# Kernel optimization log

Measured on AMD Instinct MI355X. Metric: run time of the kernel, lower is better.

The kernel has to match this reference:

```python
import jax, jax.numpy as jnp
import numpy as np
from jax import lax

# ---------- patch unfold/fold for kernel k = 2*stride (CP1: k=4,s=2; CP2: k=16,s=8) ----------

def _unfold2(x, s):
    # extract (2s x 2s) patches, stride s, VALID; x: [b,c,H,W] with H,W multiples of s
    b, c, H, W = x.shape
    nh, nw = H // s - 1, W // s - 1
    xv = x.reshape(b, c, H // s, s, W // s, s)
    quads = jnp.stack([xv[:, :, qh:qh + nh, :, qw:qw + nw, :]
                       for qh in (0, 1) for qw in (0, 1)], axis=2)
    # (b,c,q,nh,u,nw,v) -> (b,nh,nw,c,q,u,v)
    p = quads.transpose(0, 3, 5, 1, 2, 4, 6)
    return p.reshape(b, nh * nw, c * 4 * s * s), (nh, nw)


def _fold2(contrib, nh, nw, c, s):
    # overlap-add inverse of _unfold2; contrib: [b, nh*nw, c*4*s*s]
    b = contrib.shape[0]
    cr = contrib.reshape(b, nh, nw, c, 2, 2, s, s)
    out = jnp.zeros((b, c, nh + 1, s, nw + 1, s), contrib.dtype)
    for qh in (0, 1):
        for qw in (0, 1):
            blk = cr[:, :, :, :, qh, qw].transpose(0, 3, 1, 4, 2, 5)  # [b,c,nh,s,nw,s]
            out = out.at[:, :, qh:qh + nh, :, qw:qw + nw, :].add(blk)
    return out.reshape(b, c, (nh + 1) * s, (nw + 1) * s)

# ---------- gated conv (gen_conv2) / nearest-up + gated conv (gen_deconv2) ----------

def _gconv(x, w, b, stride=1, act='elu'):
    k = w.shape[-1]
    p = (k - 1) // 2
    y = lax.conv_general_dilated(x, w, (stride, stride), [(p, p), (p, p)],
                                 dimension_numbers=('NCHW', 'OIHW', 'NCHW'))
    y = y + b[None, :, None, None]
    if w.shape[0] == 3 or act is None:
        return y
    a, g = jnp.split(y, 2, axis=1)
    a = jax.nn.relu(a) if act == 'relu' else jax.nn.elu(a)
    return a * jax.nn.sigmoid(g)


def _gdeconv(x, w, b):
    x = jnp.repeat(jnp.repeat(x, 2, axis=2), 2, axis=3)  # nearest x2
    return _gconv(x, w, b)

# ---------- CP1: patch cosine-correlation + softmax matching ----------

def _cp1(x1, x2, mask, pd=1, s=2, scale=10.0):
    pads = ((0, 0), (0, 0), (pd, pd), (pd, pd))
    q, (nh, nw) = _unfold2(jnp.pad(x1, pads), s)   # [b,L,P] query patches
    kpat, _ = _unfold2(jnp.pad(x2, pads), s)       # [b,L,P] background (key) patches
    mpat, _ = _unfold2(jnp.pad(mask, pads), s)     # [b,L,4*s*s]
    kn = kpat / jnp.maximum(jnp.linalg.norm(kpat, axis=-1, keepdims=True), 1e-4)
    mm = (jnp.mean(mpat, axis=-1) == 0.).astype(x1.dtype)  # 1 = fully-known bkg patch
    cos = jnp.einsum('bqp,blp->blq', q, kn) * mm[:, :, None]
    sim = jax.nn.softmax(cos * scale, axis=1) * mm[:, :, None]
    b = x1.shape[0]
    return sim.reshape(b, nh * nw, nh, nw)

# ---------- CP2: weighted patch paste (transposed-conv reconstruction) ----------

def _cp2(sim, xb, mask, pd=4, s=8):
    b, c, H, W = xb.shape
    w, (nh, nw) = _unfold2(jnp.pad(xb, ((0, 0), (0, 0), (pd, pd), (pd, pd))), s)
    L = nh * nw
    simf = sim.reshape(b, L, L)                       # [b, L_key, L_query]
    contrib = jnp.einsum('blq,blp->bqp', simf, w)     # weighted patch per query loc
    out = _fold2(contrib, nh, nw, c, s)
    cnt = _fold2(jnp.ones((b, L, 4 * s * s), xb.dtype), nh, nw, 1, s)
    out = out / jnp.maximum(cnt, 1e-8)                # overlap average
    out = out[:, :, pd:pd + H, pd:pd + W]
    return out * mask + xb * (1. - mask)


def setup_inputs() -> dict:
    key = jax.random.key(0)
    ks = iter(jax.random.split(key, 64))
    B, H, W, cnum = 4, 256, 256, 48
    x = jax.random.uniform(next(ks), (B, 3, H, W), jnp.float32, -1., 1.)
    x_stage1 = jax.random.uniform(next(ks), (B, 3, H, W), jnp.float32, -1., 1.)
    x_stage2 = jax.random.uniform(next(ks), (B, 3, H, W), jnp.float32, -1., 1.)
    mask = jnp.zeros((B, 1, H, W), jnp.float32).at[:, :, 64:192, 64:192].set(1.)  # box hole
    pm = jax.random.normal(next(ks), (B, 2 * cnum, H // 4, W // 4), jnp.float32)
    inp = dict(x=x, mask=mask, x_stage1=x_stage1, x_stage2=x_stage2, pm=pm)
    specs = [('sconv1', 4 * cnum, 2 * cnum, 5), ('sconv2', 4 * cnum, 2 * cnum, 3),
             ('bconv1', cnum, 3, 5), ('bconv2', 2 * cnum, cnum // 2, 3),
             ('bconv3', 2 * cnum, cnum, 3), ('bconv4', 4 * cnum, cnum, 3),
             ('conv13', 2 * cnum, 2 * cnum, 3), ('conv14', 2 * cnum, 2 * cnum, 3),
             ('conv15', cnum, cnum, 3), ('conv16', cnum, cnum, 3),
             ('conv16_2', cnum, cnum // 2, 3), ('conv17', 3, cnum // 2, 3)]
    for name, cout, cin, kk in specs:
        inp['w_' + name] = jax.random.normal(next(ks), (cout, cin, kk, kk), jnp.float32) * 0.05
        inp['b_' + name] = jnp.zeros((cout,), jnp.float32)
    return inp


def reference(x, mask, x_stage1, x_stage2, pm,
              w_sconv1, b_sconv1, w_sconv2, b_sconv2,
              w_bconv1, b_bconv1, w_bconv2, b_bconv2,
              w_bconv3, b_bconv3, w_bconv4, b_bconv4,
              w_conv13, b_conv13, w_conv14, b_conv14,
              w_conv15, b_conv15, w_conv16, b_conv16,
              w_conv16_2, b_conv16_2, w_conv17, b_conv17):
    xnow = x_stage2 * mask + x * (1. - mask)
    xs = _gconv(pm, w_sconv1, b_sconv1)                       # [B,96,64,64]
    x_similar = _gconv(xs, w_sconv2, b_sconv2, act='relu')    # [B,96,64,64]
    B, _, Hm, Wm = mask.shape
    mask_s = mask.reshape(B, 1, Hm // 4, 4, Wm // 4, 4).mean(axis=(3, 5))  # avg_pool 4x4
    similar = _cp1(x_similar, x_similar, mask_s)              # [B,1024,32,32]
    xb = _gconv(xnow, w_bconv1, b_bconv1)
    skip1 = xb
    xb = _gconv(xb, w_bconv2, b_bconv2, stride=2)
    xb = _gconv(xb, w_bconv3, b_bconv3)
    skip2 = xb
    xb = _gconv(xb, w_bconv4, b_bconv4, stride=2)
    xb = _gdeconv(xb, w_conv13, b_conv13)
    xb = _gconv(jnp.concatenate([xb, skip2], axis=1), w_conv14, b_conv14)
    xb = _gdeconv(xb, w_conv15, b_conv15)
    xb = _gconv(jnp.concatenate([xb, skip1], axis=1), w_conv16, b_conv16)
    xb = _cp2(similar, xb, mask)                              # [B,24,256,256]
    xb = _gconv(xb, w_conv16_2, b_conv16_2)
    xb = jnp.tanh(_gconv(xb, w_conv17, b_conv17, act=None))
    return (x_stage1, x_stage2, xb)
```

## Files before the change

kernel.cpp:

```cpp
#include <hip/hip_runtime.h>
#include <math.h>

#define BB 4

typedef __bf16 bf16x8 __attribute__((ext_vector_type(8)));
typedef float f32x4 __attribute__((ext_vector_type(4)));

__device__ inline ushort f2bf(float x) {
  uint u = __float_as_uint(x);
  uint r = (u + 0x7fffu + ((u >> 16) & 1u)) >> 16;
  return (ushort)r;
}
__device__ inline float bf2f(ushort h) { return __uint_as_float(((uint)h) << 16); }
__device__ inline bf16x8 as_bf(uint4 u) {
  union { uint4 u; bf16x8 b; } c;
  c.u = u;
  return c.b;
}

struct WPtrs { const float* w[12]; };

#define WTOTAL 146560

__global__ void prep_w_all(WPtrs wp, uint4* __restrict__ wbH) {
  const int tK[12]    = {5,3,5,3,3,3,3,3,3,3,3,3};
  const int tCC[12]   = {8,16,8,8,16,8,16,16,16,16,8,8};
  const int tSP[12]   = {28,10,28,12,10,12,10,10,10,10,12,12};
  const int tcinR[12] = {96,96,3,24,48,48,96,96,48,48,24,24};
  const int tcinp[12] = {96,96,8,24,48,48,96,96,48,48,24,24};
  const int tcout[12] = {96,96,24,48,48,96,48,48,24,24,24,3};
  const int tgat[12]  = {1,1,1,1,1,1,1,1,1,1,1,0};
  const int toff[13]  = {0,64512,87552,89344,92800,98560,112384,123904,135424,139264,143104,145408,146560};
  for (int i = blockIdx.x * 256 + threadIdx.x; i < WTOTAL; i += gridDim.x * 256) {
    int L = 0;
    while (toff[L + 1] <= i) L++;
    int li = i - toff[L];
    int K = tK[L], CC = tCC[L], SPAD = tSP[L];
    int CH = CC >> 3;
    int SZ = SPAD * CH * 32;
    int nch = tcinp[L] / CC;
    int yb = li / (nch * SZ);
    int rem = li - yb * nch * SZ;
    int chunk = rem / SZ;
    int t = rem - chunk * SZ;
    int ci0 = chunk * CC;
    int co32 = t & 31, sh = t >> 5;
    int s = sh / CH, hh = sh - s * CH;
    int fr;
    bool ok;
    if (tgat[L]) {
      int coL = yb * 16 + (co32 & 15);
      ok = coL < tcout[L];
      fr = (co32 < 16) ? coL : tcout[L] + coL;
    } else {
      fr = yb * 32 + co32;
      ok = fr < tcout[L];
    }
    ok = ok && (s < K * K);
    const float* wgt = wp.w[L];
    union { ushort u[8]; uint4 v; } th;
#pragma unroll
    for (int j = 0; j < 8; j++) {
      int ci = ci0 + hh * 8 + j;
      float v = 0.f;
      if (ok && ci < tcinR[L]) v = wgt[((size_t)fr * tcinR[L] + ci) * (K * K) + s];
      th.u[j] = f2bf(v);
    }
    wbH[i] = th.v;
  }
}

__global__ void k_xnow(const float* __restrict__ x, const float* __restrict__ x2,
                       const float* __restrict__ mask,
                       ushort* __restrict__ outH, ushort* __restrict__ outL) {
  int idx = blockIdx.x * 256 + threadIdx.x;
  if (idx >= BB * 65536) return;
  int b = idx >> 16, r = idx & 65535;
  float m = mask[idx];
  union { ushort u[8]; uint4 v; } h, l;
#pragma unroll
  for (int c = 0; c < 8; c++) { h.u[c] = 0; l.u[c] = 0; }
#pragma unroll
  for (int c = 0; c < 3; c++) {
    size_t s = ((size_t)(b * 3 + c) << 16) + r;
    float v = x2[s] * m + x[s] * (1.f - m);
    ushort hh = f2bf(v);
    h.u[c] = hh;
    l.u[c] = f2bf(v - bf2f(hh));
  }
  *(uint4*)&outH[(size_t)idx * 8] = h.v;
  *(uint4*)&outL[(size_t)idx * 8] = l.v;
}

__global__ void k_tr(const float* __restrict__ pm,
                     ushort* __restrict__ outH, ushort* __restrict__ outL) {
  int idx = blockIdx.x * 256 + threadIdx.x;
  if (idx >= BB * 4096) return;
  int b = idx >> 12, pix = idx & 4095;
#pragma unroll
  for (int g = 0; g < 12; g++) {
    union { ushort u[8]; uint4 v; } h, l;
#pragma unroll
    for (int j = 0; j < 8; j++) {
      float v = pm[(((size_t)b * 96 + g * 8 + j) << 12) + pix];
      ushort hh = f2bf(v);
      h.u[j] = hh;
      l.u[j] = f2bf(v - bf2f(hh));
    }
    *(uint4*)&outH[(size_t)idx * 96 + g * 8] = h.v;
    *(uint4*)&outL[(size_t)idx * 96 + g * 8] = l.v;
  }
}

template <int K, int STRIDE, int UP, int CC, int TH, int TW, int SPAD>
__global__ __launch_bounds__(256) void conv_mfma(
    const ushort* __restrict__ in1H, const ushort* __restrict__ in1L,
    const ushort* __restrict__ in2H, const ushort* __restrict__ in2L,
    int s1, int s2, int g1, int cinp,
    const uint4* __restrict__ wbH,
    const float* __restrict__ bias,
    ushort* __restrict__ outH, ushort* __restrict__ outL, float* __restrict__ outF,
    int Hin, int Win, int Hout, int Wout,
    int coutEff, int coutp, int act, int tilesX) {
  constexpr int CH = CC / 8;
  constexpr int GS = 4 / CH;
  constexpr int NGc = CC / 8;
  constexpr int CCp = (CC == 16) ? 24 : 8;
  constexpr int IH = (TH - 1) * STRIDE + K;
  constexpr int IW = (TW - 1) * STRIDE + K;
  constexpr int NF = (TH * TW) / 64;
  constexpr int NSC = SPAD / GS;
  constexpr int WSZ = SPAD * CH * 32;

  __shared__ ushort sInH[IH * IW * CCp];
  __shared__ ushort sInL[IH * IW * CCp];
  __shared__ uint4 sWH[WSZ];

  const int tid = threadIdx.x;
  const int lane = tid & 63, wv = tid >> 6;
  const int m = lane & 15, gg = lane >> 4;
  const int b = blockIdx.z;
  const int yb = blockIdx.y;
  const int tX = blockIdx.x % tilesX, tY = blockIdx.x / tilesX;
  const int pad = (K - 1) / 2;
  const int HinU = Hin << UP, WinU = Win << UP;
  const int oy0 = tY * TH * STRIDE - pad;
  const int ox0 = tX * TW * STRIDE - pad;
  const int gated = (act != 2);
  const int NG = cinp >> 3;
  const int nch = cinp / CC;
  const size_t HWin = (size_t)Hin * Win;

  f32x4 acc[2][NF];
#pragma unroll
  for (int i = 0; i < 2; i++)
#pragma unroll
    for (int j = 0; j < NF; j++) acc[i][j] = (f32x4){0.f, 0.f, 0.f, 0.f};

  for (int ci0 = 0; ci0 < cinp; ci0 += CC) {
    __syncthreads();
    for (int t = tid; t < IH * IW * NGc; t += 256) {
      int p = (NGc == 2) ? (t >> 1) : t;
      int g = (NGc == 2) ? (t & 1) : 0;
      int iy = p / IW, ix = p % IW;
      int gy = oy0 + iy, gx = ox0 + ix;
      int gi = (ci0 >> 3) + g;
      uint4 h = {0u, 0u, 0u, 0u}, l = {0u, 0u, 0u, 0u};
      if (gi < NG && gy >= 0 && gy < HinU && gx >= 0 && gx < WinU) {
        int sy = gy >> UP, sx = gx >> UP;
        size_t poff = (size_t)b * HWin + (size_t)sy * Win + sx;
        if (gi < g1) {
          size_t a = poff * s1 + gi * 8;
          h = *(const uint4*)&in1H[a];
          l = *(const uint4*)&in1L[a];
        } else {
          size_t a = poff * s2 + (gi - g1) * 8;
          h = *(const uint4*)&in2H[a];
          l = *(const uint4*)&in2L[a];
        }
      }
      int d = p * CCp + g * 8;
      *(uint4*)&sInH[d] = h;
      *(uint4*)&sInL[d] = l;
    }
    {
      const uint4* pH = wbH + ((size_t)yb * nch + (ci0 / CC)) * WSZ;
      for (int t = tid; t < WSZ; t += 256) sWH[t] = pH[t];
    }
    __syncthreads();
#pragma unroll
    for (int sc = 0; sc < NSC; sc++) {
      int sg = sc * GS + gg / CH;
      int hh = gg - (gg / CH) * CH;
      int s = (sg < K * K) ? sg : 0;
      int kh = s / K, kw = s - kh * K;
      bf16x8 ah[2], bh[NF], bl[NF];
#pragma unroll
      for (int mi = 0; mi < 2; mi++) {
        int ai = (sc * 4 + gg) * 32 + mi * 16 + m;
        ah[mi] = as_bf(sWH[ai]);
      }
#pragma unroll
      for (int ni = 0; ni < NF; ni++) {
        int pix = wv * (NF * 16) + ni * 16 + m;
        int py = pix >> 4, px = pix & 15;
        int li = ((py * STRIDE + kh) * IW + px * STRIDE + kw) * CCp + hh * 8;
        bh[ni] = as_bf(*(const uint4*)&sInH[li]);
        bl[ni] = as_bf(*(const uint4*)&sInL[li]);
      }
#pragma unroll
      for (int mi = 0; mi < 2; mi++)
#pragma unroll
        for (int ni = 0; ni < NF; ni++) {
          acc[mi][ni] = __builtin_amdgcn_mfma_f32_16x16x32_bf16(ah[mi], bh[ni], acc[mi][ni], 0, 0, 0);
          acc[mi][ni] = __builtin_amdgcn_mfma_f32_16x16x32_bf16(ah[mi], bl[ni], acc[mi][ni], 0, 0, 0);
        }
    }
  }
  const size_t HWout = (size_t)Hout * Wout;
  if (gated) {
    int co0 = yb * 16 + gg * 4;
    bool cov = co0 < coutEff;
    float bA[4], bG[4];
#pragma unroll
    for (int r = 0; r < 4; r++) {
      bA[r] = cov ? bias[co0 + r] : 0.f;
      bG[r] = cov ? bias[coutEff + co0 + r] : 0.f;
    }
#pragma unroll
    for (int ni = 0; ni < NF; ni++) {
      int pix = wv * (NF * 16) + ni * 16 + m;
      int py = pix >> 4, px = pix & 15;
      int gy = tY * TH + py, gx = tX * TW + px;
      if (!cov) continue;
      union { ushort u[4]; uint2 v; } oh, ol;
#pragma unroll
      for (int r = 0; r < 4; r++) {
        float a = acc[0][ni][r] + bA[r];
        float g = acc[1][ni][r] + bG[r];
        float aa = (act == 1) ? fmaxf(a, 0.f) : (a > 0.f ? a : expm1f(a));
        float o = aa * (1.f / (1.f + expf(-g)));
        ushort hh = f2bf(o);
        oh.u[r] = hh;
        ol.u[r] = f2bf(o - bf2f(hh));
      }
      size_t base = ((size_t)b * HWout + (size_t)gy * Wout + gx) * coutp + co0;
      *(uint2*)&outH[base] = oh.v;
      *(uint2*)&outL[base] = ol.v;
    }
  } else {
#pragma unroll
    for (int mi = 0; mi < 2; mi++)
#pragma unroll
      for (int ni = 0; ni < NF; ni++) {
        int pix = wv * (NF * 16) + ni * 16 + m;
        int py = pix >> 4, px = pix & 15;
        int gy = tY * TH + py, gx = tX * TW + px;
#pragma unroll
        for (int r = 0; r < 4; r++) {
          int co = yb * 32 + mi * 16 + gg * 4 + r;
          if (co >= coutEff) continue;
          float o = tanhf(acc[mi][ni][r] + bias[co]);
          outF[(size_t)(b * coutEff + co) * HWout + (size_t)gy * Wout + gx] = o;
        }
      }
  }
}

__global__ void k_mask_s(const float* __restrict__ mask, float* __restrict__ mask_s) {
  int idx = blockIdx.x * 256 + threadIdx.x;
  if (idx >= BB * 4096) return;
  int b = idx >> 12, r = idx & 4095;
  int i = r >> 6, j = r & 63;
  float s = 0.f;
  for (int u = 0; u < 4; u++)
    for (int v = 0; v < 4; v++)
      s += mask[(size_t)b * 65536 + (i * 4 + u) * 256 + (j * 4 + v)];
  mask_s[idx] = s * (1.f / 16.f);
}

__global__ void k_mm(const float* __restrict__ mask_s, float* __restrict__ mm) {
  int idx = blockIdx.x * 256 + threadIdx.x;
  if (idx >= BB * 1024) return;
  int b = idx >> 10, l = idx & 1023;
  int li = l >> 5, lj = l & 31;
  float s = 0.f;
  for (int dy = 0; dy < 4; dy++) {
    int row = 2 * li + dy - 1;
    if (row < 0 || row >= 64) continue;
    for (int dx = 0; dx < 4; dx++) {
      int col = 2 * lj + dx - 1;
      if (col < 0 || col >= 64) continue;
      s += mask_s[((size_t)b << 12) + row * 64 + col];
    }
  }
  mm[idx] = (s == 0.f) ? 1.f : 0.f;
}

__global__ __launch_bounds__(256) void extract_patches_bf(
    const ushort* __restrict__ xsH, const ushort* __restrict__ xsL,
    ushort* __restrict__ Phi, ushort* __restrict__ Plo) {
  int bl = blockIdx.x;
  int b = bl >> 10, l = bl & 1023;
  int li = l >> 5, lj = l & 31;
  __shared__ ushort sH[1536], sL[1536];
  int tid = threadIdx.x;
  for (int t = tid; t < 192; t += 256) {
    ((uint4*)sH)[t] = (uint4){0u, 0u, 0u, 0u};
    ((uint4*)sL)[t] = (uint4){0u, 0u, 0u, 0u};
  }
  __syncthreads();
  if (tid < 192) {
    int px = tid / 12, g = tid % 12;
    int dy = px >> 2, dx = px & 3;
    int row = 2 * li + dy - 1, col = 2 * lj + dx - 1;
    if (row >= 0 && row < 64 && col >= 0 && col < 64) {
      size_t a = ((((size_t)b << 12) + (row << 6) + col) * 96) + g * 8;
      union { uint4 v; ushort u[8]; } h, lo;
      h.v = *(const uint4*)&xsH[a];
      lo.v = *(const uint4*)&xsL[a];
#pragma unroll
      for (int j = 0; j < 8; j++) {
        int c = g * 8 + j;
        sH[c * 16 + px] = h.u[j];
        sL[c * 16 + px] = lo.u[j];
      }
    }
  }
  __syncthreads();
  size_t o = (size_t)bl * 1536;
  for (int t = tid; t < 192; t += 256) {
    ((uint4*)(Phi + o))[t] = ((uint4*)sH)[t];
    ((uint4*)(Plo + o))[t] = ((uint4*)sL)[t];
  }
}

__global__ void k_scale_bf(const ushort* __restrict__ Phi, const ushort* __restrict__ Plo,
                           const float* __restrict__ mm, float* __restrict__ scale) {
  int bl = blockIdx.x;
  const ushort* rh = Phi + (size_t)bl * 1536;
  const ushort* rl = Plo + (size_t)bl * 1536;
  int tid = threadIdx.x;
  float s = 0.f;
  for (int i = 0; i < 6; i++) {
    float v = bf2f(rh[tid + i * 256]) + bf2f(rl[tid + i * 256]);
    s += v * v;
  }
  __shared__ float red[256];
  red[tid] = s; __syncthreads();
  for (int t = 128; t > 0; t >>= 1) { if (tid < t) red[tid] += red[tid + t]; __syncthreads(); }
  if (tid == 0) scale[bl] = mm[bl] / fmaxf(sqrtf(red[0]), 1e-4f);
}

__global__ __launch_bounds__(512) void gemm_qk_mfma(
    const ushort* __restrict__ Phi, const ushort* __restrict__ Plo,
    const float* __restrict__ scale, float* __restrict__ S) {
  int b = blockIdx.z;
  int qTile = blockIdx.y * 128, lTile = blockIdx.x * 128;
  __shared__ uint4 sAh[512], sAl[512], sBh[512], sBl[512];

  int tid = threadIdx.x;
  int lane = tid & 63, w = tid >> 6;
  int wy = w >> 2, wx = w & 3;
  int m = lane & 15, gg = lane >> 4;

  f32x4 acc[4][2];
#pragma unroll
  for (int i = 0; i < 4; i++)
#pragma unroll
    for (int j = 0; j < 2; j++) acc[i][j] = (f32x4){0.f, 0.f, 0.f, 0.f};

  for (int k0 = 0; k0 < 1536; k0 += 32) {
    __syncthreads();
    {
      int r = tid >> 2, g = tid & 3;
      int slot = (r << 2) + (g ^ ((r >> 1) & 3));
      size_t aoff = ((size_t)(b * 1024 + qTile + r)) * 1536 + k0;
      size_t boff = ((size_t)(b * 1024 + lTile + r)) * 1536 + k0;
      sAh[slot] = ((const uint4*)(Phi + aoff))[g];
      sAl[slot] = ((const uint4*)(Plo + aoff))[g];
      sBh[slot] = ((const uint4*)(Phi + boff))[g];
      sBl[slot] = ((const uint4*)(Plo + boff))[g];
    }
    __syncthreads();
    bf16x8 ah[4], al[4], bh[2], bl[2];
#pragma unroll
    for (int i = 0; i < 4; i++) {
      int ra = wy * 64 + i * 16 + m;
      int sa = (ra << 2) + (gg ^ ((ra >> 1) & 3));
      ah[i] = as_bf(sAh[sa]);
      al[i] = as_bf(sAl[sa]);
    }
#pragma unroll
    for (int j = 0; j < 2; j++) {
      int rb = wx * 32 + j * 16 + m;
      int sb = (rb << 2) + (gg ^ ((rb >> 1) & 3));
      bh[j] = as_bf(sBh[sb]);
      bl[j] = as_bf(sBl[sb]);
    }
#pragma unroll
    for (int mi = 0; mi < 4; mi++)
#pragma unroll
      for (int ni = 0; ni < 2; ni++) {
        acc[mi][ni] = __builtin_amdgcn_mfma_f32_16x16x32_bf16(ah[mi], bh[ni], acc[mi][ni], 0, 0, 0);
        acc[mi][ni] = __builtin_amdgcn_mfma_f32_16x16x32_bf16(ah[mi], bl[ni], acc[mi][ni], 0, 0, 0);
        acc[mi][ni] = __builtin_amdgcn_mfma_f32_16x16x32_bf16(al[mi], bh[ni], acc[mi][ni], 0, 0, 0);
      }
  }

#pragma unroll
  for (int ni = 0; ni < 2; ni++) {
    int l = lTile + wx * 32 + ni * 16 + m;
    float sc = scale[b * 1024 + l];
#pragma unroll
    for (int mi = 0; mi < 4; mi++) {
      int q0 = qTile + wy * 64 + mi * 16 + gg * 4;
#pragma unroll
      for (int r = 0; r < 4; r++)
        S[((size_t)b * 1024 + q0 + r) * 1024 + l] = acc[mi][ni][r] * sc;
    }
  }
}

__global__ void softmax_rows_bf(const float* __restrict__ S, const float* __restrict__ mm,
                                ushort* __restrict__ Shi, ushort* __restrict__ Slo) {
  int q = blockIdx.x, b = blockIdx.y;
  const float* row = S + ((size_t)b * 1024 + q) * 1024;
  int tid = threadIdx.x;
  float v[4];
  float mx = -1e30f;
  for (int i = 0; i < 4; i++) { v[i] = row[tid + i * 256]; mx = fmaxf(mx, v[i]); }
  __shared__ float red[256];
  red[tid] = mx; __syncthreads();
  for (int s = 128; s > 0; s >>= 1) { if (tid < s) red[tid] = fmaxf(red[tid], red[tid + s]); __syncthreads(); }
  mx = red[0]; __syncthreads();
  float sum = 0.f;
  for (int i = 0; i < 4; i++) { v[i] = expf(10.f * (v[i] - mx)); sum += v[i]; }
  red[tid] = sum; __syncthreads();
  for (int s = 128; s > 0; s >>= 1) { if (tid < s) red[tid] += red[tid + s]; __syncthreads(); }
  sum = red[0];
  float inv = 1.f / sum;
  for (int i = 0; i < 4; i++) {
    int l = tid + i * 256;
    float p = v[i] * inv * mm[b * 1024 + l];
    ushort h = f2bf(p);
    size_t o = ((size_t)b * 1024 + q) * 1024 + l;
    Shi[o] = h;
    Slo[o] = f2bf(p - bf2f(h));
  }
}

__global__ __launch_bounds__(256) void k_prepW(
    const ushort* __restrict__ t16H,
    ushort* __restrict__ WtH, int b) {
  int u = blockIdx.x >> 5, li = blockIdx.x & 31;
  int row = 8 * li + u - 4;
  bool rv = (row >= 0 && row < 256);
  __shared__ ushort sH[256 * 24];
  int tid = threadIdx.x;
  for (int t = tid; t < 768; t += 256) {
    uint4 h = {0u, 0u, 0u, 0u};
    if (rv) h = *(const uint4*)&t16H[((size_t)b * 65536 + (row << 8)) * 24 + t * 8];
    ((uint4*)sH)[t] = h;
  }
  __syncthreads();
  for (int pr = tid; pr < 384; pr += 256) {
    int v = pr / 24, c = pr - (pr / 24) * 24;
    int p = (u * 16 + v) * 24 + c;
    union { ushort us[32]; uint4 q[4]; } oh;
#pragma unroll 8
    for (int lj = 0; lj < 32; lj++) {
      int col = 8 * lj + v - 4;
      oh.us[lj] = (col >= 0 && col < 256) ? sH[col * 24 + c] : (ushort)0;
    }
    size_t o = (size_t)p * 1024 + li * 32;
#pragma unroll
    for (int g = 0; g < 4; g++) *(uint4*)&WtH[o + g * 8] = oh.q[g];
  }
}

__global__ __launch_bounds__(512) void gemm_cp2_mfma(
    const ushort* __restrict__ Shi, const ushort* __restrict__ Slo,
    const ushort* __restrict__ Wthi,
    float* __restrict__ contrib, int b) {
  int qTile = blockIdx.y * 128, pTile = blockIdx.x * 128;
  __shared__ uint4 sAh[512], sAl[512], sBh[512];

  int tid = threadIdx.x;
  int lane = tid & 63, w = tid >> 6;
  int wy = w >> 2, wx = w & 3;
  int m = lane & 15, gg = lane >> 4;

  f32x4 acc[4][2];
#pragma unroll
  for (int i = 0; i < 4; i++)
#pragma unroll
    for (int j = 0; j < 2; j++) acc[i][j] = (f32x4){0.f, 0.f, 0.f, 0.f};

  for (int l0 = 0; l0 < 1024; l0 += 32) {
    __syncthreads();
    {
      int r = tid >> 2, g = tid & 3;
      int slot = (r << 2) + (g ^ ((r >> 1) & 3));
      size_t aoff = ((size_t)(b * 1024 + qTile + r)) * 1024 + l0;
      size_t boff = ((size_t)(pTile + r)) * 1024 + l0;
      sAh[slot] = ((const uint4*)(Shi + aoff))[g];
      sAl[slot] = ((const uint4*)(Slo + aoff))[g];
      sBh[slot] = ((const uint4*)(Wthi + boff))[g];
    }
    __syncthreads();
    bf16x8 ah[4], al[4], bh[2];
#pragma unroll
    for (int i = 0; i < 4; i++) {
      int ra = wy * 64 + i * 16 + m;
      int sa = (ra << 2) + (gg ^ ((ra >> 1) & 3));
      ah[i] = as_bf(sAh[sa]);
      al[i] = as_bf(sAl[sa]);
    }
#pragma unroll
    for (int j = 0; j < 2; j++) {
      int rb = wx * 32 + j * 16 + m;
      int sb = (rb << 2) + (gg ^ ((rb >> 1) & 3));
      bh[j] = as_bf(sBh[sb]);
    }
#pragma unroll
    for (int mi = 0; mi < 4; mi++)
#pragma unroll
      for (int ni = 0; ni < 2; ni++) {
        acc[mi][ni] = __builtin_amdgcn_mfma_f32_16x16x32_bf16(ah[mi], bh[ni], acc[mi][ni], 0, 0, 0);
        acc[mi][ni] = __builtin_amdgcn_mfma_f32_16x16x32_bf16(al[mi], bh[ni], acc[mi][ni], 0, 0, 0);
      }
  }

#pragma unroll
  for (int ni = 0; ni < 2; ni++) {
    int p = pTile + wx * 32 + ni * 16 + m;
#pragma unroll
    for (int mi = 0; mi < 4; mi++) {
      int q0 = qTile + wy * 64 + mi * 16 + gg * 4;
#pragma unroll
      for (int r = 0; r < 4; r++)
        contrib[(size_t)(q0 + r) * 6144 + p] = acc[mi][ni][r];
    }
  }
}

__global__ void k_fold(const float* __restrict__ contrib,
                       const ushort* __restrict__ t16H, const ushort* __restrict__ t16L,
                       const float* __restrict__ mask,
                       ushort* __restrict__ outH, ushort* __restrict__ outL, int b) {
  int r = blockIdx.x * 256 + threadIdx.x;
  if (r >= 65536) return;
  int Y = r >> 8, X = r & 255;
  int yp = Y + 4, xp = X + 4;
  int qis[2], qjs[2];
  int cy = 0, cx = 0;
  int qi1 = yp >> 3;
  if (qi1 - 1 >= 0) qis[cy++] = qi1 - 1;
  if (qi1 < 32) qis[cy++] = qi1;
  int qj1 = xp >> 3;
  if (qj1 - 1 >= 0) qjs[cx++] = qj1 - 1;
  if (qj1 < 32) qjs[cx++] = qj1;
  float sum[24];
#pragma unroll
  for (int c = 0; c < 24; c++) sum[c] = 0.f;
  for (int a = 0; a < cy; a++)
    for (int d = 0; d < cx; d++) {
      int qi = qis[a], qj = qjs[d];
      int u = yp - 8 * qi, v = xp - 8 * qj;
      const float4* cp = (const float4*)&contrib[(size_t)(qi * 32 + qj) * 6144 + (u * 16 + v) * 24];
#pragma unroll
      for (int g = 0; g < 6; g++) {
        float4 f = cp[g];
        sum[g * 4 + 0] += f.x;
        sum[g * 4 + 1] += f.y;
        sum[g * 4 + 2] += f.z;
        sum[g * 4 + 3] += f.w;
      }
    }
  float inv = 1.f / (float)(cy * cx);
  float m = mask[(size_t)b * 65536 + r];
  size_t a16 = ((size_t)b * 65536 + r) * 24;
#pragma unroll
  for (int g = 0; g < 3; g++) {
    union { uint4 v; ushort u[8]; } th, tl, oh, ol;
    th.v = *(const uint4*)&t16H[a16 + g * 8];
    tl.v = *(const uint4*)&t16L[a16 + g * 8];
#pragma unroll
    for (int j = 0; j < 8; j++) {
      float base = bf2f(th.u[j]) + bf2f(tl.u[j]);
      float res = sum[g * 8 + j] * inv * m + base * (1.f - m);
      ushort h = f2bf(res);
      oh.u[j] = h;
      ol.u[j] = f2bf(res - bf2f(h));
    }
    *(uint4*)&outH[a16 + g * 8] = oh.v;
    *(uint4*)&outL[a16 + g * 8] = ol.v;
  }
}

extern "C" void kernel_launch(void* const* d_in, const int* in_sizes, int n_in,
                              void* d_out, int out_size, void* d_ws, size_t ws_size,
                              hipStream_t stream) {
  const float* x      = (const float*)d_in[0];
  const float* mask   = (const float*)d_in[1];
  const float* x_st1  = (const float*)d_in[2];
  const float* x_st2  = (const float*)d_in[3];
  const float* pm     = (const float*)d_in[4];
  const float* b_sconv1 = (const float*)d_in[6];
  const float* b_sconv2 = (const float*)d_in[8];
  const float* b_bconv1 = (const float*)d_in[10];
  const float* b_bconv2 = (const float*)d_in[12];
  const float* b_bconv3 = (const float*)d_in[14];
  const float* b_bconv4 = (const float*)d_in[16];
  const float* b_conv13 = (const float*)d_in[18];
  const float* b_conv14 = (const float*)d_in[20];
  const float* b_conv15 = (const float*)d_in[22];
  const float* b_conv16 = (const float*)d_in[24];
  const float* b_conv16_2 = (const float*)d_in[26];
  const float* b_conv17 = (const float*)d_in[28];
  float* out = (float*)d_out;
  float* ws = (float*)d_ws;
  (void)in_sizes; (void)n_in; (void)out_size; (void)ws_size;

  const size_t o_masks  = 0;
  const size_t o_mm     = 16384;
  const size_t o_scale  = 20480;
  const size_t o_xnowH  = 24576;
  const size_t o_xnowL  = 1073152;
  const size_t o_pmH    = 2121728;
  const size_t o_pmL    = 2908160;
  const size_t o_xsH    = 3694592;
  const size_t o_xsL    = 4481024;
  const size_t o_xsimH  = 5267456;
  const size_t o_xsimL  = 6053888;
  const size_t o_Phi    = 6840320;
  const size_t o_Plo    = 9986048;
  const size_t o_S      = 13131776;
  const size_t o_Shi    = 17326080;
  const size_t o_Slo    = 19423232;
  const size_t o_skip1H = 21520384;
  const size_t o_skip1L = 24666112;
  const size_t o_t2H    = 27811840;
  const size_t o_t2L    = 29384704;
  const size_t o_skip2H = 30957568;
  const size_t o_skip2L = 32530432;
  const size_t o_t4H    = 34103296;
  const size_t o_t4L    = 34889728;
  const size_t o_t13H   = 35676160;
  const size_t o_t13L   = 37249024;
  const size_t o_wbH    = 38821888;
  const size_t o_t14H = o_t2H, o_t14L = o_t2L;
  const size_t o_t15H = o_Phi, o_t15L = o_Plo;
  const size_t o_t16H = o_S;
  const size_t o_t16L = o_pmH;
  const size_t o_WtH  = o_t2H;
  const size_t o_contrib = o_Phi;
  const size_t o_cp2H = o_skip1H, o_cp2L = o_skip1L;
  const size_t o_t162H = o_Phi, o_t162L = o_Plo;

  ushort* xnowH = (ushort*)(ws + o_xnowH); ushort* xnowL = (ushort*)(ws + o_xnowL);
  ushort* pmH  = (ushort*)(ws + o_pmH);   ushort* pmL  = (ushort*)(ws + o_pmL);
  ushort* xsH  = (ushort*)(ws + o_xsH);   ushort* xsL  = (ushort*)(ws + o_xsL);
  ushort* xsimH= (ushort*)(ws + o_xsimH); ushort* xsimL= (ushort*)(ws + o_xsimL);
  ushort* Phi  = (ushort*)(ws + o_Phi);   ushort* Plo  = (ushort*)(ws + o_Plo);
  ushort* Shi  = (ushort*)(ws + o_Shi);   ushort* Slo  = (ushort*)(ws + o_Slo);
  ushort* skip1H=(ushort*)(ws + o_skip1H);ushort* skip1L=(ushort*)(ws + o_skip1L);
  ushort* t2H  = (ushort*)(ws + o_t2H);   ushort* t2L  = (ushort*)(ws + o_t2L);
  ushort* skip2H=(ushort*)(ws + o_skip2H);ushort* skip2L=(ushort*)(ws + o_skip2L);
  ushort* t4H  = (ushort*)(ws + o_t4H);   ushort* t4L  = (ushort*)(ws + o_t4L);
  ushort* t13H = (ushort*)(ws + o_t13H);  ushort* t13L = (ushort*)(ws + o_t13L);
  ushort* t14H = (ushort*)(ws + o_t14H);  ushort* t14L = (ushort*)(ws + o_t14L);
  ushort* t15H = (ushort*)(ws + o_t15H);  ushort* t15L = (ushort*)(ws + o_t15L);
  ushort* t16H = (ushort*)(ws + o_t16H);  ushort* t16L = (ushort*)(ws + o_t16L);
  ushort* WtH  = (ushort*)(ws + o_WtH);
  ushort* cp2H = (ushort*)(ws + o_cp2H);  ushort* cp2L = (ushort*)(ws + o_cp2L);
  ushort* t162H= (ushort*)(ws + o_t162H); ushort* t162L= (ushort*)(ws + o_t162L);
  uint4* wbH = (uint4*)(ws + o_wbH);

  const size_t LOFF[12] = {0, 64512, 87552, 89344, 92800, 98560,
                           112384, 123904, 135424, 139264, 143104, 145408};

  WPtrs wp;
  wp.w[0] = (const float*)d_in[5];   wp.w[1] = (const float*)d_in[7];
  wp.w[2] = (const float*)d_in[9];   wp.w[3] = (const float*)d_in[11];
  wp.w[4] = (const float*)d_in[13];  wp.w[5] = (const float*)d_in[15];
  wp.w[6] = (const float*)d_in[17];  wp.w[7] = (const float*)d_in[19];
  wp.w[8] = (const float*)d_in[21];  wp.w[9] = (const float*)d_in[23];
  wp.w[10] = (const float*)d_in[25]; wp.w[11] = (const float*)d_in[27];
  prep_w_all<<<128, 256, 0, stream>>>(wp, wbH);

  hipMemcpyAsync(out, x_st1, (size_t)786432 * 4, hipMemcpyDeviceToDevice, stream);
  hipMemcpyAsync(out + 786432, x_st2, (size_t)786432 * 4, hipMemcpyDeviceToDevice, stream);

  k_xnow<<<1024, 256, 0, stream>>>(x, x_st2, mask, xnowH, xnowL);
  k_tr<<<64, 256, 0, stream>>>(pm, pmH, pmL);

  conv_mfma<5, 1, 0, 8, 16, 16, 28><<<dim3(16, 6, BB), 256, 0, stream>>>(
      pmH, pmL, nullptr, nullptr, 96, 0, 12, 96, wbH + LOFF[0], b_sconv1,
      xsH, xsL, nullptr, 64, 64, 64, 64, 96, 96, 0, 4);
  conv_mfma<3, 1, 0, 16, 16, 16, 10><<<dim3(16, 6, BB), 256, 0, stream>>>(
      xsH, xsL, nullptr, nullptr, 96, 0, 12, 96, wbH + LOFF[1], b_sconv2,
      xsimH, xsimL, nullptr, 64, 64, 64, 64, 96, 96, 1, 4);
  k_mask_s<<<64, 256, 0, stream>>>(mask, ws + o_masks);
  k_mm<<<16, 256, 0, stream>>>(ws + o_masks, ws + o_mm);
  extract_patches_bf<<<4096, 256, 0, stream>>>(xsimH, xsimL, Phi, Plo);
  k_scale_bf<<<4096, 256, 0, stream>>>(Phi, Plo, ws + o_mm, ws + o_scale);
  gemm_qk_mfma<<<dim3(8, 8, BB), 512, 0, stream>>>(Phi, Plo, ws + o_scale, ws + o_S);
  softmax_rows_bf<<<dim3(1024, BB), 256, 0, stream>>>(ws + o_S, ws + o_mm, Shi, Slo);

  conv_mfma<5, 1, 0, 8, 16, 16, 28><<<dim3(256, 2, BB), 256, 0, stream>>>(
      xnowH, xnowL, nullptr, nullptr, 8, 0, 1, 8, wbH + LOFF[2], b_bconv1,
      skip1H, skip1L, nullptr, 256, 256, 256, 256, 24, 24, 0, 16);
  conv_mfma<3, 2, 0, 8, 8, 16, 12><<<dim3(128, 3, BB), 256, 0, stream>>>(
      skip1H, skip1L, nullptr, nullptr, 24, 0, 3, 24, wbH + LOFF[3], b_bconv2,
      t2H, t2L, nullptr, 256, 256, 128, 128, 48, 48, 0, 8);
  conv_mfma<3, 1, 0, 16, 16, 16, 10><<<dim3(64, 3, BB), 256, 0, stream>>>(
      t2H, t2L, nullptr, nullptr, 48, 0, 6, 48, wbH + LOFF[4], b_bconv3,
      skip2H, skip2L, nullptr, 128, 128, 128, 128, 48, 48, 0, 8);
  conv_mfma<3, 2, 0, 8, 8, 16, 12><<<dim3(32, 6, BB), 256, 0, stream>>>(
      skip2H, skip2L, nullptr, nullptr, 48, 0, 6, 48, wbH + LOFF[5], b_bconv4,
      t4H, t4L, nullptr, 128, 128, 64, 64, 96, 96, 0, 4);
  conv_mfma<3, 1, 1, 16, 16, 16, 10><<<dim3(64, 3, BB), 256, 0, stream>>>(
      t4H, t4L, nullptr, nullptr, 96, 0, 12, 96, wbH + LOFF[6], b_conv13,
      t13H, t13L, nullptr, 64, 64, 128, 128, 48, 48, 0, 8);
  conv_mfma<3, 1, 0, 16, 16, 16, 10><<<dim3(64, 3, BB), 256, 0, stream>>>(
      t13H, t13L, skip2H, skip2L, 48, 48, 6, 96, wbH + LOFF[7], b_conv14,
      t14H, t14L, nullptr, 128, 128, 128, 128, 48, 48, 0, 8);
  conv_mfma<3, 1, 1, 16, 16, 16, 10><<<dim3(256, 2, BB), 256, 0, stream>>>(
      t14H, t14L, nullptr, nullptr, 48, 0, 6, 48, wbH + LOFF[8], b_conv15,
      t15H, t15L, nullptr, 128, 128, 256, 256, 24, 24, 0, 16);
  conv_mfma<3, 1, 0, 16, 16, 16, 10><<<dim3(256, 2, BB), 256, 0, stream>>>(
      t15H, t15L, skip1H, skip1L, 24, 24, 3, 48, wbH + LOFF[9], b_conv16,
      t16H, t16L, nullptr, 256, 256, 256, 256, 24, 24, 0, 16);

  for (int b = 0; b < BB; b++) {
    k_prepW<<<512, 256, 0, stream>>>(t16H, WtH, b);
    gemm_cp2_mfma<<<dim3(48, 8), 512, 0, stream>>>(Shi, Slo, WtH, ws + o_contrib, b);
    k_fold<<<256, 256, 0, stream>>>(ws + o_contrib, t16H, t16L, mask, cp2H, cp2L, b);
  }

  conv_mfma<3, 1, 0, 8, 16, 16, 12><<<dim3(256, 2, BB), 256, 0, stream>>>(
      cp2H, cp2L, nullptr, nullptr, 24, 0, 3, 24, wbH + LOFF[10], b_conv16_2,
      t162H, t162L, nullptr, 256, 256, 256, 256, 24, 24, 0, 16);
  conv_mfma<3, 1, 0, 8, 16, 16, 12><<<dim3(256, 1, BB), 256, 0, stream>>>(
      t162H, t162L, nullptr, nullptr, 24, 0, 3, 24, wbH + LOFF[11], b_conv17,
      nullptr, nullptr, out + 2 * 786432, 256, 256, 256, 256, 3, 24, 2, 16);
}
```

Baseline: 860.7 us.

## Deepen K-tiles and widen CP2 GEMM tile with grouped block ordering

Both split-bf16 MFMA GEMMs now stage 64-wide K slices per shared-memory round instead of 32, which halves the number of barriers, and use a new XOR swizzle over 8 column groups. The CP2 GEMM grows its output tile to 128x256 (4x4 accumulators per wave) so each A tile is reused across twice as many columns, and its grid is halved. Block indices are remapped so consecutive blocks sweep the query tiles first, meant to improve L2 reuse of the shared operand. The costs are more shared memory and more registers per block, which may lower occupancy, and a CP2 grid of only 192 blocks per batch.

```diff
diff --git a/kernel.cpp b/kernel.cpp
--- a/kernel.cpp
+++ b/kernel.cpp
@@ -356,8 +356,9 @@
     const ushort* __restrict__ Phi, const ushort* __restrict__ Plo,
     const float* __restrict__ scale, float* __restrict__ S) {
   int b = blockIdx.z;
-  int qTile = blockIdx.y * 128, lTile = blockIdx.x * 128;
-  __shared__ uint4 sAh[512], sAl[512], sBh[512], sBl[512];
+  int f = blockIdx.x + (blockIdx.y << 3);
+  int qTile = (f & 7) * 128, lTile = (f >> 3) * 128;
+  __shared__ uint4 sAh[1024], sAl[1024], sBh[1024], sBl[1024];
 
   int tid = threadIdx.x;
   int lane = tid & 63, w = tid >> 6;
@@ -370,11 +371,11 @@
 #pragma unroll
     for (int j = 0; j < 2; j++) acc[i][j] = (f32x4){0.f, 0.f, 0.f, 0.f};
 
-  for (int k0 = 0; k0 < 1536; k0 += 32) {
+  for (int k0 = 0; k0 < 1536; k0 += 64) {
     __syncthreads();
-    {
-      int r = tid >> 2, g = tid & 3;
-      int slot = (r << 2) + (g ^ ((r >> 1) & 3));
+    for (int t = tid; t < 1024; t += 512) {
+      int r = t >> 3, g = t & 7;
+      int slot = (r << 3) + (g ^ (r & 7));
       size_t aoff = ((size_t)(b * 1024 + qTile + r)) * 1536 + k0;
       size_t boff = ((size_t)(b * 1024 + lTile + r)) * 1536 + k0;
       sAh[slot] = ((const uint4*)(Phi + aoff))[g];
@@ -383,29 +384,32 @@
       sBl[slot] = ((const uint4*)(Plo + boff))[g];
     }
     __syncthreads();
-    bf16x8 ah[4], al[4], bh[2], bl[2];
-#pragma unroll
-    for (int i = 0; i < 4; i++) {
-      int ra = wy * 64 + i * 16 + m;
-      int sa = (ra << 2) + (gg ^ ((ra >> 1) & 3));
-      ah[i] = as_bf(sAh[sa]);
-      al[i] = as_bf(sAl[sa]);
-    }
-#pragma unroll
-    for (int j = 0; j < 2; j++) {
-      int rb = wx * 32 + j * 16 + m;
-      int sb = (rb << 2) + (gg ^ ((rb >> 1) & 3));
-      bh[j] = as_bf(sBh[sb]);
-      bl[j] = as_bf(sBl[sb]);
-    }
-#pragma unroll
-    for (int mi = 0; mi < 4; mi++)
-#pragma unroll
-      for (int ni = 0; ni < 2; ni++) {
-        acc[mi][ni] = __builtin_amdgcn_mfma_f32_16x16x32_bf16(ah[mi], bh[ni], acc[mi][ni], 0, 0, 0);
-        acc[mi][ni] = __builtin_amdgcn_mfma_f32_16x16x32_bf16(ah[mi], bl[ni], acc[mi][ni], 0, 0, 0);
-        acc[mi][ni] = __builtin_amdgcn_mfma_f32_16x16x32_bf16(al[mi], bh[ni], acc[mi][ni], 0, 0, 0);
-      }
+#pragma unroll
+    for (int c = 0; c < 2; c++) {
+      bf16x8 ah[4], al[4], bh[2], bl[2];
+#pragma unroll
+      for (int i = 0; i < 4; i++) {
+        int ra = wy * 64 + i * 16 + m;
+        int sa = (ra << 3) + ((c * 4 + gg) ^ (ra & 7));
+        ah[i] = as_bf(sAh[sa]);
+        al[i] = as_bf(sAl[sa]);
+      }
+#pragma unroll
+      for (int j = 0; j < 2; j++) {
+        int rb = wx * 32 + j * 16 + m;
+        int sb = (rb << 3) + ((c * 4 + gg) ^ (rb & 7));
+        bh[j] = as_bf(sBh[sb]);
+        bl[j] = as_bf(sBl[sb]);
+      }
+#pragma unroll
+      for (int mi = 0; mi < 4; mi++)
+#pragma unroll
+        for (int ni = 0; ni < 2; ni++) {
+          acc[mi][ni] = __builtin_amdgcn_mfma_f32_16x16x32_bf16(ah[mi], bh[ni], acc[mi][ni], 0, 0, 0);
+          acc[mi][ni] = __builtin_amdgcn_mfma_f32_16x16x32_bf16(ah[mi], bl[ni], acc[mi][ni], 0, 0, 0);
+          acc[mi][ni] = __builtin_amdgcn_mfma_f32_16x16x32_bf16(al[mi], bh[ni], acc[mi][ni], 0, 0, 0);
+        }
+    }
   }
 
 #pragma unroll
@@ -483,58 +487,66 @@
     const ushort* __restrict__ Shi, const ushort* __restrict__ Slo,
     const ushort* __restrict__ Wthi,
     float* __restrict__ contrib, int b) {
-  int qTile = blockIdx.y * 128, pTile = blockIdx.x * 128;
-  __shared__ uint4 sAh[512], sAl[512], sBh[512];
+  int f = blockIdx.x + blockIdx.y * 24;
+  int qTile = (f & 7) * 128, pTile = (f >> 3) * 256;
+  __shared__ uint4 sAh[1024], sAl[1024], sBh[2048];
 
   int tid = threadIdx.x;
   int lane = tid & 63, w = tid >> 6;
   int wy = w >> 2, wx = w & 3;
   int m = lane & 15, gg = lane >> 4;
 
-  f32x4 acc[4][2];
+  f32x4 acc[4][4];
 #pragma unroll
   for (int i = 0; i < 4; i++)
 #pragma unroll
-    for (int j = 0; j < 2; j++) acc[i][j] = (f32x4){0.f, 0.f, 0.f, 0.f};
-
-  for (int l0 = 0; l0 < 1024; l0 += 32) {
+    for (int j = 0; j < 4; j++) acc[i][j] = (f32x4){0.f, 0.f, 0.f, 0.f};
+
+  for (int l0 = 0; l0 < 1024; l0 += 64) {
     __syncthreads();
-    {
-      int r = tid >> 2, g = tid & 3;
-      int slot = (r << 2) + (g ^ ((r >> 1) & 3));
+    for (int t = tid; t < 1024; t += 512) {
+      int r = t >> 3, g = t & 7;
+      int slot = (r << 3) + (g ^ (r & 7));
       size_t aoff = ((size_t)(b * 1024 + qTile + r)) * 1024 + l0;
-      size_t boff = ((size_t)(pTile + r)) * 1024 + l0;
       sAh[slot] = ((const uint4*)(Shi + aoff))[g];
       sAl[slot] = ((const uint4*)(Slo + aoff))[g];
+    }
+    for (int t = tid; t < 2048; t += 512) {
+      int r = t >> 3, g = t & 7;
+      int slot = (r << 3) + (g ^ (r & 7));
+      size_t boff = ((size_t)(pTile + r)) * 1024 + l0;
       sBh[slot] = ((const uint4*)(Wthi + boff))[g];
     }
     __syncthreads();
-    bf16x8 ah[4], al[4], bh[2];
-#pragma unroll
-    for (int i = 0; i < 4; i++) {
-      int ra = wy * 64 + i * 16 + m;
-      int sa = (ra << 2) + (gg ^ ((ra >> 1) & 3));
-      ah[i] = as_bf(sAh[sa]);
-      al[i] = as_bf(sAl[sa]);
-    }
-#pragma unroll
-    for (int j = 0; j < 2; j++) {
-      int rb = wx * 32 + j * 16 + m;
-      int sb = (rb << 2) + (gg ^ ((rb >> 1) & 3));
-      bh[j] = as_bf(sBh[sb]);
-    }
-#pragma unroll
-    for (int mi = 0; mi < 4; mi++)
-#pragma unroll
-      for (int ni = 0; ni < 2; ni++) {
-        acc[mi][ni] = __builtin_amdgcn_mfma_f32_16x16x32_bf16(ah[mi], bh[ni], acc[mi][ni], 0, 0, 0);
-        acc[mi][ni] = __builtin_amdgcn_mfma_f32_16x16x32_bf16(al[mi], bh[ni], acc[mi][ni], 0, 0, 0);
-      }
-  }
-
-#pragma unroll
-  for (int ni = 0; ni < 2; ni++) {
-    int p = pTile + wx * 32 + ni * 16 + m;
+#pragma unroll
+    for (int c = 0; c < 2; c++) {
+      bf16x8 ah[4], al[4], bh[4];
+#pragma unroll
+      for (int i = 0; i < 4; i++) {
+        int ra = wy * 64 + i * 16 + m;
+        int sa = (ra << 3) + ((c * 4 + gg) ^ (ra & 7));
+        ah[i] = as_bf(sAh[sa]);
+        al[i] = as_bf(sAl[sa]);
+      }
+#pragma unroll
+      for (int j = 0; j < 4; j++) {
+        int rb = wx * 64 + j * 16 + m;
+        int sb = (rb << 3) + ((c * 4 + gg) ^ (rb & 7));
+        bh[j] = as_bf(sBh[sb]);
+      }
+#pragma unroll
+      for (int mi = 0; mi < 4; mi++)
+#pragma unroll
+        for (int ni = 0; ni < 4; ni++) {
+          acc[mi][ni] = __builtin_amdgcn_mfma_f32_16x16x32_bf16(ah[mi], bh[ni], acc[mi][ni], 0, 0, 0);
+          acc[mi][ni] = __builtin_amdgcn_mfma_f32_16x16x32_bf16(al[mi], bh[ni], acc[mi][ni], 0, 0, 0);
+        }
+    }
+  }
+
+#pragma unroll
+  for (int ni = 0; ni < 4; ni++) {
+    int p = pTile + wx * 64 + ni * 16 + m;
 #pragma unroll
     for (int mi = 0; mi < 4; mi++) {
       int q0 = qTile + wy * 64 + mi * 16 + gg * 4;
@@ -736,7 +748,7 @@
 
   for (int b = 0; b < BB; b++) {
     k_prepW<<<512, 256, 0, stream>>>(t16H, WtH, b);
-    gemm_cp2_mfma<<<dim3(48, 8), 512, 0, stream>>>(Shi, Slo, WtH, ws + o_contrib, b);
+    gemm_cp2_mfma<<<dim3(24, 8), 512, 0, stream>>>(Shi, Slo, WtH, ws + o_contrib, b);
     k_fold<<<256, 256, 0, stream>>>(ws + o_contrib, t16H, t16L, mask, cp2H, cp2L, b);
   }
 
```

After: 962.3 us. 11.8% more time.
